# Performance work log

Hardware: AMD Instinct MI355X
Metric: run time of the kernel (lower is better)

## Reference

```python
import jax, jax.numpy as jnp
import numpy as np

PARTS, BATCH, SEQ, DP = 5, 128, 300, 30   # parts, batch, seq_len, per-part feat dim
HID, CLASSES = 512, 60
IN = PARTS * DP                            # input_size = 150


def setup_inputs() -> dict:
    key = jax.random.key(0)
    ks = jax.random.split(key, 9)
    s = lambda *d: 1.0 / np.sqrt(d[-2])
    return {
        "inputs": jax.random.normal(ks[0], (PARTS, BATCH, SEQ, DP), jnp.float32),
        # per-part gate weights (i, f, g stacked along last dim -> 3H)
        "Wx": jax.random.normal(ks[1], (PARTS, DP, 3 * HID), jnp.float32) * (1.0 / np.sqrt(DP)),
        "Wh": jax.random.normal(ks[2], (PARTS, HID, 3 * HID), jnp.float32) * (1.0 / np.sqrt(HID)),
        "b": jax.random.normal(ks[3], (PARTS, 3 * HID), jnp.float32) * 0.01,
        # shared output gate over full input + hidden
        "Wxo": jax.random.normal(ks[4], (IN, HID), jnp.float32) * (1.0 / np.sqrt(IN)),
        "Who": jax.random.normal(ks[5], (HID, HID), jnp.float32) * (1.0 / np.sqrt(HID)),
        "bo": jax.random.normal(ks[6], (HID,), jnp.float32) * 0.01,
        # classifier
        "fc_w": jax.random.normal(ks[7], (HID, CLASSES), jnp.float32) * (1.0 / np.sqrt(HID)),
        "fc_b": jax.random.normal(ks[8], (CLASSES,), jnp.float32) * 0.01,
    }


def reference(inputs, Wx, Wh, b, Wxo, Who, bo, fc_w, fc_b):
    # Part-aware LSTM (NTU RGB+D): each body part has its own i/f/g gates and
    # cell state; a shared output gate acts on the concatenated input.
    P, B, T, D = inputs.shape
    H = Wh.shape[1]
    x_seq = jnp.transpose(inputs, (2, 1, 0, 3))  # [T, B, P, D]

    h0 = jnp.zeros((B, H), inputs.dtype)
    c0 = jnp.zeros((B, P, H), inputs.dtype)     # torch stores this flattened [B, P*H]

    def step(carry, x_t):                        # x_t: [B, P, D]
        h, c = carry
        gates = (jnp.einsum('bpd,pdg->bpg', x_t, Wx)
                 + jnp.einsum('bh,phg->bpg', h, Wh) + b)   # [B, P, 3H]
        i, f, g = jnp.split(gates, 3, axis=-1)
        c_new = jax.nn.sigmoid(f) * c + jax.nn.sigmoid(i) * jnp.tanh(g)
        x_flat = x_t.reshape(B, P * D)                     # concat of parts
        o = jax.nn.sigmoid(x_flat @ Wxo + h @ Who + bo)    # shared output gate
        h_new = o * jnp.tanh(c_new.sum(axis=1))            # aggregate part cells
        return (h_new, c_new), None

    (hT, _), _ = jax.lax.scan(step, (h0, c0), x_seq)
    logits = hT @ fc_w + fc_b
    return jax.nn.log_softmax(logits, axis=-1)
```

## Files before the change

### kernel.cpp

```cpp
#include <hip/hip_runtime.h>

typedef unsigned short u16;
typedef unsigned int   u32;
typedef unsigned long long u64;
typedef __attribute__((ext_vector_type(8))) short bf16x8;
typedef __attribute__((ext_vector_type(16))) float f32x16;
typedef __attribute__((ext_vector_type(4))) float f32x4;
typedef __attribute__((ext_vector_type(4))) u32 u32x4;

#define T_SEQ 300

#define OFF_WP   0u
#define OFF_BP   11010048u
#define OFF_XB   11042816u
#define OFF_H    25788416u
#define OFF_FL   65241088u

__device__ __forceinline__ float bf2f(u16 u){ union { u32 u; float f; } v; v.u = ((u32)u) << 16; return v.f; }
__device__ __forceinline__ u16 f2bf(float f){
  union { float f; u32 u; } v; v.f = f;
  u32 r = v.u + 0x7fffu + ((v.u >> 16) & 1u);
  return (u16)(r >> 16);
}
__device__ __forceinline__ float sigf(float x){ return 1.f / (1.f + __expf(-x)); }
__device__ __forceinline__ float tanh_f(float x){ return 1.f - 2.f / (1.f + __expf(2.f * x)); }

__global__ void prep(const float* __restrict__ Wx, const float* __restrict__ Wh,
                     const float* __restrict__ bg, const float* __restrict__ Wxo,
                     const float* __restrict__ Who, const float* __restrict__ bo,
                     u16* __restrict__ Wp, float* __restrict__ bpack,
                     u16* __restrict__ h0, int* __restrict__ flags)
{
  int w = blockIdx.x * 256 + threadIdx.x;

  if (w < 8192) {
    u32x4 z = {0u, 0u, 0u, 0u};
    ((u32x4*)h0)[w] = z;
    int j = w >> 4, g = w & 15;
    float bv;
    if (g < 15) { int p = g / 3, t3 = g - p * 3; bv = bg[p * 1536 + t3 * 512 + j]; }
    else bv = bo[j];
    bpack[w] = bv;
  }
  if (w < 128) flags[w] = 0;

  int lane = w & 63, rem = w >> 6;
  int kk = rem % 42, jp = rem / 42;
  int m = lane & 31, hi = lane >> 5;
  int jj = (m >> 2) & 1, g = (m & 3) + 4 * (m >> 3);
  int j = jp * 2 + jj;
  union { u16 s[8]; u32x4 v; } o;
  #pragma unroll
  for (int i = 0; i < 8; ++i) {
    int k = kk * 16 + hi * 8 + i;
    float val = 0.f;
    if (g < 15) {
      int p = g / 3, t3 = g - p * 3, col = t3 * 512 + j;
      if (k < 512) val = Wh[(p * 512 + k) * 1536 + col];
      else {
        int s = k - 512, px = s >> 5, cc = (s >> 3) & 3, ii = s & 7;
        int d = (cc < 3) ? cc * 8 + ii : ((ii < 2) ? -1 : 22 + ii);
        if (px == p && d >= 0) val = Wx[(p * 30 + d) * 1536 + col];
      }
    } else {
      if (k < 512) val = Who[k * 512 + j];
      else {
        int s = k - 512, px = s >> 5, cc = (s >> 3) & 3, ii = s & 7;
        int d = (cc < 3) ? cc * 8 + ii : ((ii < 2) ? -1 : 22 + ii);
        if (d >= 0) val = Wxo[(px * 30 + d) * 512 + j];
      }
    }
    o.s[i] = f2bf(val);
  }
  *(u32x4*)(Wp + ((size_t)(jp * 42 + kk) * 64 + lane) * 8) = o.v;
}

__global__ void prep_x(const float* __restrict__ x, u16* __restrict__ xb)
{
  int w = blockIdx.x * 256 + threadIdx.x;
  int cx = w % 24, rem = w / 24;
  int bglob = rem % 128, t = rem / 128;
  union { u16 s[8]; u32x4 v; } o;
  int s0 = cx << 3;
  if (s0 >= 160) {
    u32x4 z = {0u, 0u, 0u, 0u}; o.v = z;
  } else {
    int p = s0 >> 5, cc = (s0 >> 3) & 3;
    const float* row = x + ((size_t)(p * 128 + bglob) * 300 + t) * 30;
    #pragma unroll
    for (int i = 0; i < 8; ++i) {
      int d = (cc < 3) ? cc * 8 + i : 22 + i;
      o.s[i] = f2bf(row[d]);
    }
  }
  *(u32x4*)(xb + (size_t)w * 8) = o.v;
}

__device__ __forceinline__ void wait_flags32(const int* f, int t)
{
  int l = threadIdx.x & 31;
  for (;;) {
    int v = __hip_atomic_load(&f[l], __ATOMIC_RELAXED, __HIP_MEMORY_SCOPE_AGENT);
    if (__all(v >= t)) break;
  }
}

__global__ void __launch_bounds__(512, 2)
plstm(const u16* __restrict__ xb, const u16* __restrict__ Wp,
      const float* __restrict__ bpack, u16* hall, int* flags,
      const float* __restrict__ fcw, const float* __restrict__ fcb,
      float* __restrict__ out)
{
  __shared__ __align__(16) u16 Hsh[32 * 512];
  __shared__ __align__(16) u16 Xsh[32 * 256];
  __shared__ __align__(16) u16 hbuf[32 * 16];

  const int tid  = threadIdx.x;
  const int lane = tid & 63;
  const int wv   = tid >> 6;
  const int n    = lane & 31;
  const int hi   = lane >> 5;
  const int bq   = blockIdx.x & 3;
  const int jgh  = blockIdx.x >> 2;
  const int jp   = jgh * 8 + wv;
  const int j    = jp * 2 + hi;
  int* myflags = flags + bq * 32;

  bf16x8 afr[42];
  {
    const u16* wpb = Wp + ((size_t)jp * 42 * 64 + lane) * 8;
    #pragma unroll
    for (int kk = 0; kk < 42; ++kk)
      afr[kk] = *(const bf16x8*)(wpb + kk * 512);
  }
  float bias[16];
  #pragma unroll
  for (int i = 0; i < 4; ++i)
    *(f32x4*)(bias + i * 4) = *(const f32x4*)(bpack + j * 16 + i * 4);

  float cst[5] = {0.f, 0.f, 0.f, 0.f, 0.f};

  for (int t = 0; t < T_SEQ; ++t) {
    {
      const u16* xsrc = xb + (size_t)(t * 128 + bq * 32) * 192;
      #pragma unroll
      for (int i = 0; i < 2; ++i) {
        int c = tid + (i << 9);
        if (c < 768) {
          int b = c / 24, cx = c - b * 24;
          u32x4 v = *(const u32x4*)(xsrc + b * 192 + (cx << 3));
          *(u32x4*)(Xsh + (b << 8) + (((cx ^ b) & 31) << 3)) = v;
        }
      }
    }
    __syncthreads();

    f32x16 acc;
    #pragma unroll
    for (int i = 0; i < 16; ++i) acc[i] = 0.f;

    #pragma unroll
    for (int kx = 0; kx < 10; ++kx) {
      int c = kx * 2 + hi;
      bf16x8 bf = *(const bf16x8*)(Xsh + (n << 8) + (((c ^ n) & 31) << 3));
      acc = __builtin_amdgcn_mfma_f32_32x32x16_bf16(afr[32 + kx], bf, acc, 0, 0, 0);
    }

    if (wv == 0) wait_flags32(myflags, t);
    __syncthreads();

    {
      const u16* hsrc = hall + (size_t)t * 65536 + ((bq * 32) << 9);
      #pragma unroll
      for (int i = 0; i < 4; ++i) {
        int c = (tid + (i << 9) + (jgh << 6)) & 2047;
        int b = c >> 6, cx = c & 63;
        u32x4 v = *(const u32x4*)(hsrc + (b << 9) + (cx << 3));
        int phys = (cx & 32) | ((cx ^ b) & 31);
        *(u32x4*)(Hsh + (b << 9) + (phys << 3)) = v;
      }
    }
    __syncthreads();

    #pragma unroll
    for (int kk = 0; kk < 32; ++kk) {
      int c = kk * 2 + hi;
      int phys = (c & 32) | ((c ^ n) & 31);
      bf16x8 bf = *(const bf16x8*)(Hsh + (n << 9) + (phys << 3));
      acc = __builtin_amdgcn_mfma_f32_32x32x16_bf16(afr[kk], bf, acc, 0, 0, 0);
    }

    float cs = 0.f;
    #pragma unroll
    for (int p = 0; p < 5; ++p) {
      float iv = acc[p * 3 + 0] + bias[p * 3 + 0];
      float fv = acc[p * 3 + 1] + bias[p * 3 + 1];
      float gv = acc[p * 3 + 2] + bias[p * 3 + 2];
      cst[p] = sigf(fv) * cst[p] + sigf(iv) * tanh_f(gv);
      cs += cst[p];
    }
    float hv = sigf(acc[15] + bias[15]) * tanh_f(cs);

    hbuf[(n << 4) + (wv << 1) + hi] = f2bf(hv);
    __syncthreads();
    if (tid < 64) {
      int row = tid >> 1, half = tid & 1;
      const u16* src = hbuf + (row << 4) + (half << 3);
      u64 v0 = *(const u64*)(src);
      u64 v1 = *(const u64*)(src + 4);
      u64* dst = (u64*)(hall + (size_t)(t + 1) * 65536
                        + (size_t)(bq * 32 + row) * 512 + (jgh << 4) + (half << 3));
      __hip_atomic_store(dst,     v0, __ATOMIC_RELAXED, __HIP_MEMORY_SCOPE_AGENT);
      __hip_atomic_store(dst + 1, v1, __ATOMIC_RELAXED, __HIP_MEMORY_SCOPE_AGENT);
      asm volatile("s_waitcnt vmcnt(0)" ::: "memory");
      if (tid == 0)
        __hip_atomic_store(&myflags[jgh], t + 1, __ATOMIC_RELAXED, __HIP_MEMORY_SCOPE_AGENT);
    }
  }

  if (blockIdx.x >= 64) return;
  for (;;) {
    int v0 = __hip_atomic_load(&flags[lane],      __ATOMIC_RELAXED, __HIP_MEMORY_SCOPE_AGENT);
    int v1 = __hip_atomic_load(&flags[64 + lane], __ATOMIC_RELAXED, __HIP_MEMORY_SCOPE_AGENT);
    if (__all(min(v0, v1) >= T_SEQ)) break;
  }
  __syncthreads();
  float* fsh = (float*)Hsh;
  const u16* hT = hall + (size_t)T_SEQ * 65536;
  for (int r = 0; r < 2; ++r) {
    int row = blockIdx.x * 2 + r;
    int ks = tid >> 6, c = tid & 63;
    float s = 0.f;
    if (c < 60) {
      const u16* hr = hT + row * 512 + ks * 64;
      const float* wr = fcw + (size_t)(ks * 64) * 60 + c;
      #pragma unroll 8
      for (int k = 0; k < 64; ++k) s += bf2f(hr[k]) * wr[k * 60];
    }
    __syncthreads();
    fsh[ks * 64 + c] = s;
    __syncthreads();
    if (tid < 60) {
      float lg = fcb[tid];
      #pragma unroll
      for (int i = 0; i < 8; ++i) lg += fsh[i * 64 + tid];
      fsh[512 + tid] = lg;
    }
    __syncthreads();
    if (tid == 0) {
      float mx = -1e30f;
      for (int i = 0; i < 60; ++i) mx = fmaxf(mx, fsh[512 + i]);
      float sm = 0.f;
      for (int i = 0; i < 60; ++i) sm += __expf(fsh[512 + i] - mx);
      fsh[576] = mx + __logf(sm);
    }
    __syncthreads();
    if (tid < 60) out[row * 60 + tid] = fsh[512 + tid] - fsh[576];
    __syncthreads();
  }
}

extern "C" void kernel_launch(void* const* d_in, const int* in_sizes, int n_in,
                              void* d_out, int out_size, void* d_ws, size_t ws_size,
                              hipStream_t stream)
{
  const float* xin = (const float*)d_in[0];
  const float* Wx  = (const float*)d_in[1];
  const float* Wh  = (const float*)d_in[2];
  const float* bg  = (const float*)d_in[3];
  const float* Wxo = (const float*)d_in[4];
  const float* Who = (const float*)d_in[5];
  const float* bo  = (const float*)d_in[6];
  const float* fcw = (const float*)d_in[7];
  const float* fcb = (const float*)d_in[8];
  float* out = (float*)d_out;

  char* ws = (char*)d_ws;
  u16*   Wp    = (u16*)(ws + OFF_WP);
  float* bpack = (float*)(ws + OFF_BP);
  u16*   xb    = (u16*)(ws + OFF_XB);
  u16*   hall  = (u16*)(ws + OFF_H);
  int*   flags = (int*)(ws + OFF_FL);

  hipLaunchKernelGGL(prep, dim3(2688), dim3(256), 0, stream,
                     Wx, Wh, bg, Wxo, Who, bo, Wp, bpack, hall, flags);
  hipLaunchKernelGGL(prep_x, dim3(3600), dim3(256), 0, stream, xin, xb);

  void* args[] = { (void*)&xb, (void*)&Wp, (void*)&bpack, (void*)&hall,
                   (void*)&flags, (void*)&fcw, (void*)&fcb, (void*)&out };
  hipLaunchCooperativeKernel((void*)plstm, dim3(128), dim3(512), args, 0, stream);
}
```

Measured before the change: 1.553 ms.

## Precompute next-step input gate MFMAs during flag wait and reorganize h layout

Double-buffers the staged input slice so the x-part MFMAs for step t+1 (and the load for t+2) run right after publishing h at step t, overlapping them with the cross-block flag wait. The global h buffer is re-laid out so each block writes one contiguous 1 KB chunk per batch quarter instead of strided 32-byte pieces, and the readers and final classifier gather from the new layout. The flag spin now issues two loads per iteration and is moved to wave 7. It adds an LDS buffer and raises register pressure from keeping accumulators live across the loop.

```diff
diff --git a/kernel.cpp b/kernel.cpp
--- a/kernel.cpp
+++ b/kernel.cpp
@@ -100,8 +100,10 @@
 {
   int l = threadIdx.x & 31;
   for (;;) {
-    int v = __hip_atomic_load(&f[l], __ATOMIC_RELAXED, __HIP_MEMORY_SCOPE_AGENT);
-    if (__all(v >= t)) break;
+    int v1 = __hip_atomic_load(&f[l], __ATOMIC_RELAXED, __HIP_MEMORY_SCOPE_AGENT);
+    int v2 = __hip_atomic_load(&f[l], __ATOMIC_RELAXED, __HIP_MEMORY_SCOPE_AGENT);
+    if (__all(v1 >= t)) break;
+    if (__all(v2 >= t)) break;
   }
 }
 
@@ -112,7 +114,7 @@
       float* __restrict__ out)
 {
   __shared__ __align__(16) u16 Hsh[32 * 512];
-  __shared__ __align__(16) u16 Xsh[32 * 256];
+  __shared__ __align__(16) u16 Xsh[2][32 * 256];
   __shared__ __align__(16) u16 hbuf[32 * 16];
 
   const int tid  = threadIdx.x;
@@ -140,44 +142,46 @@
 
   float cst[5] = {0.f, 0.f, 0.f, 0.f, 0.f};
 
+  auto stage_x = [&](int t, u16* dst) {
+    const u16* xsrc = xb + (size_t)(t * 128 + bq * 32) * 192;
+    #pragma unroll
+    for (int i = 0; i < 2; ++i) {
+      int c = tid + (i << 9);
+      if (c < 768) {
+        int b = c / 24, cx = c - b * 24;
+        u32x4 v = *(const u32x4*)(xsrc + b * 192 + (cx << 3));
+        *(u32x4*)(dst + (b << 8) + (((cx ^ b) & 31) << 3)) = v;
+      }
+    }
+  };
+
+  f32x16 acc;
+  #pragma unroll
+  for (int i = 0; i < 16; ++i) acc[i] = 0.f;
+
+  stage_x(0, Xsh[0]);
+  __syncthreads();
+  #pragma unroll
+  for (int kx = 0; kx < 10; ++kx) {
+    int c = kx * 2 + hi;
+    bf16x8 bf = *(const bf16x8*)(Xsh[0] + (n << 8) + (((c ^ n) & 31) << 3));
+    acc = __builtin_amdgcn_mfma_f32_32x32x16_bf16(afr[32 + kx], bf, acc, 0, 0, 0);
+  }
+  stage_x(1, Xsh[1]);
+
   for (int t = 0; t < T_SEQ; ++t) {
+    if (wv == 7) wait_flags32(myflags, t);
+    __syncthreads();
+
     {
-      const u16* xsrc = xb + (size_t)(t * 128 + bq * 32) * 192;
-      #pragma unroll
-      for (int i = 0; i < 2; ++i) {
-        int c = tid + (i << 9);
-        if (c < 768) {
-          int b = c / 24, cx = c - b * 24;
-          u32x4 v = *(const u32x4*)(xsrc + b * 192 + (cx << 3));
-          *(u32x4*)(Xsh + (b << 8) + (((cx ^ b) & 31) << 3)) = v;
-        }
-      }
-    }
-    __syncthreads();
-
-    f32x16 acc;
-    #pragma unroll
-    for (int i = 0; i < 16; ++i) acc[i] = 0.f;
-
-    #pragma unroll
-    for (int kx = 0; kx < 10; ++kx) {
-      int c = kx * 2 + hi;
-      bf16x8 bf = *(const bf16x8*)(Xsh + (n << 8) + (((c ^ n) & 31) << 3));
-      acc = __builtin_amdgcn_mfma_f32_32x32x16_bf16(afr[32 + kx], bf, acc, 0, 0, 0);
-    }
-
-    if (wv == 0) wait_flags32(myflags, t);
-    __syncthreads();
-
-    {
-      const u16* hsrc = hall + (size_t)t * 65536 + ((bq * 32) << 9);
+      const u16* hsrc = hall + (size_t)t * 65536 + bq * 16384;
       #pragma unroll
       for (int i = 0; i < 4; ++i) {
-        int c = (tid + (i << 9) + (jgh << 6)) & 2047;
-        int b = c >> 6, cx = c & 63;
-        u32x4 v = *(const u32x4*)(hsrc + (b << 9) + (cx << 3));
-        int phys = (cx & 32) | ((cx ^ b) & 31);
-        *(u32x4*)(Hsh + (b << 9) + (phys << 3)) = v;
+        int idx = (tid + (i << 9) + (jgh << 6)) & 2047;
+        int n2 = idx >> 6, c = idx & 63;
+        u32x4 v = *(const u32x4*)(hsrc + ((c >> 1) << 9) + (n2 << 4) + ((c & 1) << 3));
+        int phys = (c & 32) | ((c ^ n2) & 31);
+        *(u32x4*)(Hsh + (n2 << 9) + (phys << 3)) = v;
       }
     }
     __syncthreads();
@@ -204,17 +208,28 @@
     hbuf[(n << 4) + (wv << 1) + hi] = f2bf(hv);
     __syncthreads();
     if (tid < 64) {
-      int row = tid >> 1, half = tid & 1;
-      const u16* src = hbuf + (row << 4) + (half << 3);
+      const u16* src = hbuf + tid * 8;
       u64 v0 = *(const u64*)(src);
       u64 v1 = *(const u64*)(src + 4);
-      u64* dst = (u64*)(hall + (size_t)(t + 1) * 65536
-                        + (size_t)(bq * 32 + row) * 512 + (jgh << 4) + (half << 3));
+      u64* dst = (u64*)(hall + (size_t)(t + 1) * 65536 + bq * 16384 + jgh * 512 + tid * 8);
       __hip_atomic_store(dst,     v0, __ATOMIC_RELAXED, __HIP_MEMORY_SCOPE_AGENT);
       __hip_atomic_store(dst + 1, v1, __ATOMIC_RELAXED, __HIP_MEMORY_SCOPE_AGENT);
       asm volatile("s_waitcnt vmcnt(0)" ::: "memory");
       if (tid == 0)
         __hip_atomic_store(&myflags[jgh], t + 1, __ATOMIC_RELAXED, __HIP_MEMORY_SCOPE_AGENT);
+    }
+
+    if (t < T_SEQ - 1) {
+      #pragma unroll
+      for (int i = 0; i < 16; ++i) acc[i] = 0.f;
+      const u16* xs = Xsh[(t + 1) & 1];
+      #pragma unroll
+      for (int kx = 0; kx < 10; ++kx) {
+        int c = kx * 2 + hi;
+        bf16x8 bf = *(const bf16x8*)(xs + (n << 8) + (((c ^ n) & 31) << 3));
+        acc = __builtin_amdgcn_mfma_f32_32x32x16_bf16(afr[32 + kx], bf, acc, 0, 0, 0);
+      }
+      if (t < T_SEQ - 2) stage_x(t + 2, Xsh[t & 1]);
     }
   }
 
@@ -232,10 +247,11 @@
     int ks = tid >> 6, c = tid & 63;
     float s = 0.f;
     if (c < 60) {
-      const u16* hr = hT + row * 512 + ks * 64;
+      const u16* hb = hT + (row >> 5) * 16384 + (row & 31) * 16;
       const float* wr = fcw + (size_t)(ks * 64) * 60 + c;
       #pragma unroll 8
-      for (int k = 0; k < 64; ++k) s += bf2f(hr[k]) * wr[k * 60];
+      for (int k = 0; k < 64; ++k)
+        s += bf2f(hb[(ks * 4 + (k >> 4)) * 512 + (k & 15)]) * wr[k * 60];
     }
     __syncthreads();
     fsh[ks * 64 + c] = s;
```

Result: slower. 1.648 ms (+6.1%).

## Halve grid to 64 blocks, each handling 64 batch rows with two MFMA tiles

Applied to the files above, without the earlier changes.

Each block now processes two 32-row batch tiles (64 rows) per timestep instead of one, halving the cooperative grid from 128 to 64 blocks and the flag groups from 4 to 2. Weight fragments held in registers are reused across both tiles, and fewer blocks take part in the per-step flag synchronisation, which cuts cross-block sync cost. The trade-off is doubled per-block LDS, more register pressure from two accumulators and twice the cell state, longer serial work per step, and fewer CUs in use.

```diff
diff --git a/kernel.cpp b/kernel.cpp
--- a/kernel.cpp
+++ b/kernel.cpp
@@ -42,7 +42,7 @@
     else bv = bo[j];
     bpack[w] = bv;
   }
-  if (w < 128) flags[w] = 0;
+  if (w < 64) flags[w] = 0;
 
   int lane = w & 63, rem = w >> 6;
   int kk = rem % 42, jp = rem / 42;
@@ -111,20 +111,20 @@
       const float* __restrict__ fcw, const float* __restrict__ fcb,
       float* __restrict__ out)
 {
-  __shared__ __align__(16) u16 Hsh[32 * 512];
-  __shared__ __align__(16) u16 Xsh[32 * 256];
-  __shared__ __align__(16) u16 hbuf[32 * 16];
+  __shared__ __align__(16) u16 Hsh[64 * 512];
+  __shared__ __align__(16) u16 Xsh[64 * 256];
+  __shared__ __align__(16) u16 hbuf[64 * 16];
 
   const int tid  = threadIdx.x;
   const int lane = tid & 63;
   const int wv   = tid >> 6;
   const int n    = lane & 31;
   const int hi   = lane >> 5;
-  const int bq   = blockIdx.x & 3;
-  const int jgh  = blockIdx.x >> 2;
+  const int bh   = blockIdx.x & 1;
+  const int jgh  = blockIdx.x >> 1;
   const int jp   = jgh * 8 + wv;
   const int j    = jp * 2 + hi;
-  int* myflags = flags + bq * 32;
+  int* myflags = flags + bh * 32;
 
   bf16x8 afr[42];
   {
@@ -138,42 +138,42 @@
   for (int i = 0; i < 4; ++i)
     *(f32x4*)(bias + i * 4) = *(const f32x4*)(bpack + j * 16 + i * 4);
 
-  float cst[5] = {0.f, 0.f, 0.f, 0.f, 0.f};
+  float cst[2][5] = {{0.f,0.f,0.f,0.f,0.f},{0.f,0.f,0.f,0.f,0.f}};
 
   for (int t = 0; t < T_SEQ; ++t) {
     {
-      const u16* xsrc = xb + (size_t)(t * 128 + bq * 32) * 192;
+      const u16* xsrc = xb + (size_t)(t * 128 + bh * 64) * 192;
       #pragma unroll
-      for (int i = 0; i < 2; ++i) {
+      for (int i = 0; i < 3; ++i) {
         int c = tid + (i << 9);
-        if (c < 768) {
-          int b = c / 24, cx = c - b * 24;
-          u32x4 v = *(const u32x4*)(xsrc + b * 192 + (cx << 3));
-          *(u32x4*)(Xsh + (b << 8) + (((cx ^ b) & 31) << 3)) = v;
-        }
-      }
-    }
-    __syncthreads();
-
-    f32x16 acc;
-    #pragma unroll
-    for (int i = 0; i < 16; ++i) acc[i] = 0.f;
+        int b = c / 24, cx = c - b * 24;
+        u32x4 v = *(const u32x4*)(xsrc + b * 192 + (cx << 3));
+        *(u32x4*)(Xsh + (b << 8) + (((cx ^ b) & 31) << 3)) = v;
+      }
+    }
+    __syncthreads();
+
+    f32x16 acc0, acc1;
+    #pragma unroll
+    for (int i = 0; i < 16; ++i) { acc0[i] = 0.f; acc1[i] = 0.f; }
 
     #pragma unroll
     for (int kx = 0; kx < 10; ++kx) {
       int c = kx * 2 + hi;
-      bf16x8 bf = *(const bf16x8*)(Xsh + (n << 8) + (((c ^ n) & 31) << 3));
-      acc = __builtin_amdgcn_mfma_f32_32x32x16_bf16(afr[32 + kx], bf, acc, 0, 0, 0);
+      bf16x8 b0 = *(const bf16x8*)(Xsh + (n << 8) + (((c ^ n) & 31) << 3));
+      bf16x8 b1 = *(const bf16x8*)(Xsh + ((n + 32) << 8) + (((c ^ (n + 32)) & 31) << 3));
+      acc0 = __builtin_amdgcn_mfma_f32_32x32x16_bf16(afr[32 + kx], b0, acc0, 0, 0, 0);
+      acc1 = __builtin_amdgcn_mfma_f32_32x32x16_bf16(afr[32 + kx], b1, acc1, 0, 0, 0);
     }
 
     if (wv == 0) wait_flags32(myflags, t);
     __syncthreads();
 
     {
-      const u16* hsrc = hall + (size_t)t * 65536 + ((bq * 32) << 9);
+      const u16* hsrc = hall + (size_t)t * 65536 + ((bh * 64) << 9);
       #pragma unroll
-      for (int i = 0; i < 4; ++i) {
-        int c = (tid + (i << 9) + (jgh << 6)) & 2047;
+      for (int i = 0; i < 8; ++i) {
+        int c = (tid + (i << 9) + (jgh << 7)) & 4095;
         int b = c >> 6, cx = c & 63;
         u32x4 v = *(const u32x4*)(hsrc + (b << 9) + (cx << 3));
         int phys = (cx & 32) | ((cx ^ b) & 31);
@@ -185,44 +185,53 @@
     #pragma unroll
     for (int kk = 0; kk < 32; ++kk) {
       int c = kk * 2 + hi;
-      int phys = (c & 32) | ((c ^ n) & 31);
-      bf16x8 bf = *(const bf16x8*)(Hsh + (n << 9) + (phys << 3));
-      acc = __builtin_amdgcn_mfma_f32_32x32x16_bf16(afr[kk], bf, acc, 0, 0, 0);
-    }
-
-    float cs = 0.f;
-    #pragma unroll
-    for (int p = 0; p < 5; ++p) {
-      float iv = acc[p * 3 + 0] + bias[p * 3 + 0];
-      float fv = acc[p * 3 + 1] + bias[p * 3 + 1];
-      float gv = acc[p * 3 + 2] + bias[p * 3 + 2];
-      cst[p] = sigf(fv) * cst[p] + sigf(iv) * tanh_f(gv);
-      cs += cst[p];
-    }
-    float hv = sigf(acc[15] + bias[15]) * tanh_f(cs);
-
-    hbuf[(n << 4) + (wv << 1) + hi] = f2bf(hv);
-    __syncthreads();
+      int ph0 = (c & 32) | ((c ^ n) & 31);
+      int ph1 = (c & 32) | ((c ^ (n + 32)) & 31);
+      bf16x8 b0 = *(const bf16x8*)(Hsh + (n << 9) + (ph0 << 3));
+      bf16x8 b1 = *(const bf16x8*)(Hsh + ((n + 32) << 9) + (ph1 << 3));
+      acc0 = __builtin_amdgcn_mfma_f32_32x32x16_bf16(afr[kk], b0, acc0, 0, 0, 0);
+      acc1 = __builtin_amdgcn_mfma_f32_32x32x16_bf16(afr[kk], b1, acc1, 0, 0, 0);
+    }
+
+    #pragma unroll
+    for (int tile = 0; tile < 2; ++tile) {
+      const f32x16& a = tile ? acc1 : acc0;
+      float cs = 0.f;
+      #pragma unroll
+      for (int p = 0; p < 5; ++p) {
+        float iv = a[p * 3 + 0] + bias[p * 3 + 0];
+        float fv = a[p * 3 + 1] + bias[p * 3 + 1];
+        float gv = a[p * 3 + 2] + bias[p * 3 + 2];
+        cst[tile][p] = sigf(fv) * cst[tile][p] + sigf(iv) * tanh_f(gv);
+        cs += cst[tile][p];
+      }
+      float hv = sigf(a[15] + bias[15]) * tanh_f(cs);
+      hbuf[((tile * 32 + n) << 4) + (wv << 1) + hi] = f2bf(hv);
+    }
+    __syncthreads();
+
     if (tid < 64) {
-      int row = tid >> 1, half = tid & 1;
-      const u16* src = hbuf + (row << 4) + (half << 3);
+      const u16* src = hbuf + (tid << 4);
       u64 v0 = *(const u64*)(src);
       u64 v1 = *(const u64*)(src + 4);
+      u64 v2 = *(const u64*)(src + 8);
+      u64 v3 = *(const u64*)(src + 12);
       u64* dst = (u64*)(hall + (size_t)(t + 1) * 65536
-                        + (size_t)(bq * 32 + row) * 512 + (jgh << 4) + (half << 3));
+                        + (size_t)(bh * 64 + tid) * 512 + (jgh << 4));
       __hip_atomic_store(dst,     v0, __ATOMIC_RELAXED, __HIP_MEMORY_SCOPE_AGENT);
       __hip_atomic_store(dst + 1, v1, __ATOMIC_RELAXED, __HIP_MEMORY_SCOPE_AGENT);
+      __hip_atomic_store(dst + 2, v2, __ATOMIC_RELAXED, __HIP_MEMORY_SCOPE_AGENT);
+      __hip_atomic_store(dst + 3, v3, __ATOMIC_RELAXED, __HIP_MEMORY_SCOPE_AGENT);
       asm volatile("s_waitcnt vmcnt(0)" ::: "memory");
       if (tid == 0)
         __hip_atomic_store(&myflags[jgh], t + 1, __ATOMIC_RELAXED, __HIP_MEMORY_SCOPE_AGENT);
     }
-  }
-
-  if (blockIdx.x >= 64) return;
+    __syncthreads();
+  }
+
   for (;;) {
-    int v0 = __hip_atomic_load(&flags[lane],      __ATOMIC_RELAXED, __HIP_MEMORY_SCOPE_AGENT);
-    int v1 = __hip_atomic_load(&flags[64 + lane], __ATOMIC_RELAXED, __HIP_MEMORY_SCOPE_AGENT);
-    if (__all(min(v0, v1) >= T_SEQ)) break;
+    int v = __hip_atomic_load(&flags[lane], __ATOMIC_RELAXED, __HIP_MEMORY_SCOPE_AGENT);
+    if (__all(v >= T_SEQ)) break;
   }
   __syncthreads();
   float* fsh = (float*)Hsh;
@@ -288,5 +297,5 @@
 
   void* args[] = { (void*)&xb, (void*)&Wp, (void*)&bpack, (void*)&hall,
                    (void*)&flags, (void*)&fcw, (void*)&fcb, (void*)&out };
-  hipLaunchCooperativeKernel((void*)plstm, dim3(128), dim3(512), args, 0, stream);
-}
+  hipLaunchCooperativeKernel((void*)plstm, dim3(64), dim3(512), args, 0, stream);
+}
```

After: 2.833 ms. +82.4%, slower.

## Pad sync flags to separate cache lines and tile hidden-state buffer per block

Applied to the files above, without the earlier changes.

Each producer block's completion flag is padded to its own 128-byte slot, so polling and flag stores no longer share cache lines. The global hidden-state buffer is relaid out so each producer block writes one contiguous 1 KB chunk instead of 32 scattered 32-byte pieces. Consumers remap the chunked layout into the swizzled shared-memory tile, and the final classifier reads hT with the new indexing. The aim is to cut cross-block coherence traffic and write fragmentation on the per-timestep critical path, at the cost of more complex address arithmetic and a larger flag array.

```diff
diff --git a/kernel.cpp b/kernel.cpp
--- a/kernel.cpp
+++ b/kernel.cpp
@@ -42,7 +42,7 @@
     else bv = bo[j];
     bpack[w] = bv;
   }
-  if (w < 128) flags[w] = 0;
+  if (w < 4096) flags[w] = 0;
 
   int lane = w & 63, rem = w >> 6;
   int kk = rem % 42, jp = rem / 42;
@@ -100,7 +100,7 @@
 {
   int l = threadIdx.x & 31;
   for (;;) {
-    int v = __hip_atomic_load(&f[l], __ATOMIC_RELAXED, __HIP_MEMORY_SCOPE_AGENT);
+    int v = __hip_atomic_load(&f[l * 32], __ATOMIC_RELAXED, __HIP_MEMORY_SCOPE_AGENT);
     if (__all(v >= t)) break;
   }
 }
@@ -124,7 +124,7 @@
   const int jgh  = blockIdx.x >> 2;
   const int jp   = jgh * 8 + wv;
   const int j    = jp * 2 + hi;
-  int* myflags = flags + bq * 32;
+  int* myflags = flags + bq * 1024;
 
   bf16x8 afr[42];
   {
@@ -170,14 +170,15 @@
     __syncthreads();
 
     {
-      const u16* hsrc = hall + (size_t)t * 65536 + ((bq * 32) << 9);
+      const u16* hsrc = hall + (size_t)t * 65536 + bq * 16384;
       #pragma unroll
       for (int i = 0; i < 4; ++i) {
-        int c = (tid + (i << 9) + (jgh << 6)) & 2047;
-        int b = c >> 6, cx = c & 63;
-        u32x4 v = *(const u32x4*)(hsrc + (b << 9) + (cx << 3));
-        int phys = (cx & 32) | ((cx ^ b) & 31);
-        *(u32x4*)(Hsh + (b << 9) + (phys << 3)) = v;
+        int idx = (tid + (i << 9) + (jgh << 6)) & 2047;
+        u32x4 v = *(const u32x4*)(hsrc + idx * 8);
+        int nn = (idx >> 1) & 31;
+        int cx = ((idx >> 6) << 1) | (idx & 1);
+        int phys = (cx & 32) | ((cx ^ nn) & 31);
+        *(u32x4*)(Hsh + (nn << 9) + (phys << 3)) = v;
       }
     }
     __syncthreads();
@@ -204,24 +205,23 @@
     hbuf[(n << 4) + (wv << 1) + hi] = f2bf(hv);
     __syncthreads();
     if (tid < 64) {
-      int row = tid >> 1, half = tid & 1;
-      const u16* src = hbuf + (row << 4) + (half << 3);
+      const u16* src = hbuf + tid * 8;
       u64 v0 = *(const u64*)(src);
       u64 v1 = *(const u64*)(src + 4);
-      u64* dst = (u64*)(hall + (size_t)(t + 1) * 65536
-                        + (size_t)(bq * 32 + row) * 512 + (jgh << 4) + (half << 3));
+      u64* dst = (u64*)(hall + (size_t)(t + 1) * 65536 + bq * 16384
+                        + jgh * 512 + tid * 8);
       __hip_atomic_store(dst,     v0, __ATOMIC_RELAXED, __HIP_MEMORY_SCOPE_AGENT);
       __hip_atomic_store(dst + 1, v1, __ATOMIC_RELAXED, __HIP_MEMORY_SCOPE_AGENT);
       asm volatile("s_waitcnt vmcnt(0)" ::: "memory");
       if (tid == 0)
-        __hip_atomic_store(&myflags[jgh], t + 1, __ATOMIC_RELAXED, __HIP_MEMORY_SCOPE_AGENT);
+        __hip_atomic_store(&myflags[jgh * 32], t + 1, __ATOMIC_RELAXED, __HIP_MEMORY_SCOPE_AGENT);
     }
   }
 
   if (blockIdx.x >= 64) return;
   for (;;) {
-    int v0 = __hip_atomic_load(&flags[lane],      __ATOMIC_RELAXED, __HIP_MEMORY_SCOPE_AGENT);
-    int v1 = __hip_atomic_load(&flags[64 + lane], __ATOMIC_RELAXED, __HIP_MEMORY_SCOPE_AGENT);
+    int v0 = __hip_atomic_load(&flags[lane * 32],        __ATOMIC_RELAXED, __HIP_MEMORY_SCOPE_AGENT);
+    int v1 = __hip_atomic_load(&flags[2048 + lane * 32], __ATOMIC_RELAXED, __HIP_MEMORY_SCOPE_AGENT);
     if (__all(min(v0, v1) >= T_SEQ)) break;
   }
   __syncthreads();
@@ -232,10 +232,11 @@
     int ks = tid >> 6, c = tid & 63;
     float s = 0.f;
     if (c < 60) {
-      const u16* hr = hT + row * 512 + ks * 64;
+      const u16* hb = hT + (row >> 5) * 16384 + (row & 31) * 16;
       const float* wr = fcw + (size_t)(ks * 64) * 60 + c;
       #pragma unroll 8
-      for (int k = 0; k < 64; ++k) s += bf2f(hr[k]) * wr[k * 60];
+      for (int k = 0; k < 64; ++k)
+        s += bf2f(hb[(ks * 4 + (k >> 4)) * 512 + (k & 15)]) * wr[k * 60];
     }
     __syncthreads();
     fsh[ks * 64 + c] = s;
```

After: 1.489 ms. 1.04x faster.
